# Kernel optimization log

Measured on AMD Instinct MI355X. Metric: run time of the kernel, lower is better.

## Reference

```python
import jax, jax.numpy as jnp
import numpy as np

B, T, HID = 2, 2048, 1024
NH = 8
QK_DIM = 1024
V_DIM = 2048
SCALE_BASE = 512.0
GN_EPS = 1e-5


def _xpos_rotate(x, downscale):
    # x: [B, T, QK_DIM]; XPOS rotary embedding (syncdoth/RetNet, offset=0)
    d = QK_DIM
    dh = d // 2
    pos = jnp.arange(T, dtype=jnp.float32)
    # per-pair magnitude scale
    base_scale = (jnp.arange(0, d, 2, dtype=jnp.float32) + 0.4 * d) / (1.4 * d)  # [dh]
    scale = base_scale[None, :] ** (pos[:, None] / SCALE_BASE)  # [T, dh]
    if downscale:
        scale = 1.0 / scale
    inv_freq = 1.0 / (10000.0 ** (jnp.arange(dh, dtype=jnp.float32) / dh))
    sinusoid = pos[:, None] * inv_freq[None, :]  # [T, dh]
    sin = jnp.sin(sinusoid) * scale
    cos = jnp.cos(sinusoid) * scale
    # duplicate_interleave -> [T, d]
    sin = jnp.repeat(sin, 2, axis=-1)
    cos = jnp.repeat(cos, 2, axis=-1)
    x1 = x[..., 0::2]
    x2 = x[..., 1::2]
    rot = jnp.stack((-x2, x1), axis=-1).reshape(x.shape)  # rotate_every_two
    return x * cos[None] + rot * sin[None]


def setup_inputs() -> dict:
    key = jax.random.key(0)
    k1, k2, k3, k4 = jax.random.split(key, 4)
    x = jax.random.normal(k1, (B, T, HID), dtype=jnp.float32)
    Wqkv = jax.random.normal(k2, (HID, 2 * QK_DIM + V_DIM), dtype=jnp.float32) / np.sqrt(HID)
    Wg = jax.random.normal(k3, (HID, V_DIM), dtype=jnp.float32) / np.sqrt(HID)
    Wp = jax.random.normal(k4, (V_DIM, HID), dtype=jnp.float32) / np.sqrt(V_DIM)
    bp = jnp.zeros((HID,), dtype=jnp.float32)
    return {"x": x, "Wqkv": Wqkv, "Wg": Wg, "Wp": Wp, "bp": bp}


def reference(x, Wqkv, Wg, Wp, bp):
    # multi-scale decay (non-default gamma path)
    gamma = 1.0 - jnp.exp(jnp.linspace(np.log(1.0 / 32), np.log(1.0 / 512), NH)).astype(jnp.float32)  # [NH]

    qkv = x @ Wqkv  # [B,T,2qk+v]
    q, k, v = jnp.split(qkv, [QK_DIM, 2 * QK_DIM], axis=-1)
    q = _xpos_rotate(q, downscale=False)
    k = _xpos_rotate(k, downscale=True)

    dqk = QK_DIM // NH
    dv = V_DIM // NH
    q = q.reshape(B, T, NH, dqk).transpose(0, 2, 1, 3)  # [B,H,T,dqk]
    k = k.reshape(B, T, NH, dqk).transpose(0, 2, 1, 3)
    v = v.reshape(B, T, NH, dv).transpose(0, 2, 1, 3)   # [B,H,T,dv]

    # parallel decay mask: gamma^(i-j) for i>=j else 0  -> [H,T,T]
    idx = jnp.arange(T)
    expo = idx[:, None] - idx[None, :]
    expo_safe = jnp.where(expo >= 0, expo, 0).astype(jnp.float32)
    decay_mask = jnp.where(expo[None] >= 0, gamma[:, None, None] ** expo_safe[None], 0.0)  # [H,T,T]

    scores = jnp.einsum('bhid,bhjd->bhij', q, k) * (dqk ** -0.5)
    retention = jnp.einsum('bhij,bhjv->bhiv', scores * decay_mask[None], v)  # [B,H,T,dv]

    # current_kv state: sum_t decay_mask[h,-1,t] * k_t (outer) v_t  -> [B,H,dqk,dv]
    curr_kv = jnp.einsum('bhtk,bhtv,ht->bhkv', k, v, decay_mask[:, -1, :])

    ret = retention.transpose(0, 2, 1, 3).reshape(B, T, V_DIM)

    # GroupNorm(num_groups=NH, affine=False) over [B*T, V_DIM]
    g = ret.reshape(B, T, NH, dv)
    mu = jnp.mean(g, axis=-1, keepdims=True)
    var = jnp.var(g, axis=-1, keepdims=True)
    normed = ((g - mu) / jnp.sqrt(var + GN_EPS)).reshape(B, T, V_DIM)

    gate = jax.nn.silu(x @ Wg)
    out = (gate * normed) @ Wp + bp
    return out, curr_kv
```

## Files before the change

kernel.cpp:

```cpp
#include <hip/hip_runtime.h>

typedef unsigned short u16;
typedef unsigned int   u32;
typedef unsigned long long u64;

typedef __attribute__((ext_vector_type(8))) short bf8_t;
typedef __attribute__((ext_vector_type(4))) float f4_t;

#define DEVI __device__ __forceinline__
#define MFMA16(a,b,c) __builtin_amdgcn_mfma_f32_16x16x32_bf16((a),(b),(c),0,0,0)

#define BB   2
#define TT   2048
#define HIDN 1024
#define L0f  (-3.4657359027997265f)
#define DLf  (-0.3960841031714215f)
#define SCL  (0.08838834764831845f)

DEVI u16 f2b(float f) {
    u32 u = __float_as_uint(f);
    u += 0x7FFFu + ((u >> 16) & 1u);
    return (u16)(u >> 16);
}
DEVI float b2f(u16 u) { return __uint_as_float(((u32)u) << 16); }

DEVI void gll16(const void* g, void* l) {
    __builtin_amdgcn_global_load_lds((const __attribute__((address_space(1))) void*)g,
                                     (__attribute__((address_space(3))) void*)l, 16, 0, 0);
}

__global__ __launch_bounds__(256) void k_tables(u32* __restrict__ cqp, u32* __restrict__ ckp,
                                                float* __restrict__ gt, float* __restrict__ gk) {
    int bx = blockIdx.x;
    if (bx >= 4096) {
        int i = (bx - 4096) * 256 + threadIdx.x;
        if (i < 16384) {
            int h = i >> 11, t = i & 2047;
            float lg2 = log2f(1.f - expf(L0f + (float)h * DLf));
            gt[i] = exp2f((float)(2047 - t) * lg2);
        } else {
            int idx = i - 16384;
            int h = idx >> 6, d = idx & 63;
            float lg2 = log2f(1.f - expf(L0f + (float)h * DLf));
            gk[idx] = exp2f(-(float)d * lg2);
        }
        return;
    }
    int idx = bx * 256 + threadIdx.x;
    int t = idx >> 9, m = idx & 511;
    float base = (2.f * (float)m + 409.6f) * (1.f / 1433.6f);
    float s = exp2f(log2f(base) * ((float)t * (1.f / 512.f)));
    float invf = exp2f(-(float)m * (13.287712379549449f / 512.f));
    float sn, cs;
    sincosf((float)t * invf, &sn, &cs);
    int h = m >> 6;
    float lg2h = log2f(1.f - expf(L0f + (float)h * DLf));
    float qf = s * SCL * exp2f((float)(t & 63) * lg2h);
    cqp[idx] = (u32)f2b(cs * qf) | ((u32)f2b(sn * qf) << 16);
    float is = 1.f / s;
    ckp[idx] = (u32)f2b(cs * is) | ((u32)f2b(sn * is) << 16);
}

__global__ __launch_bounds__(256) void k_cvt(const float* __restrict__ in, u16* __restrict__ out) {
    int i = blockIdx.x * 256 + threadIdx.x;
    float4 v = ((const float4*)in)[i];
    u64 pk = (u64)f2b(v.x) | ((u64)f2b(v.y) << 16) | ((u64)f2b(v.z) << 32) | ((u64)f2b(v.w) << 48);
    ((u64*)out)[i] = pk;
}

__global__ __launch_bounds__(256) void k_tposeF(const float* __restrict__ Wqkv,
                                                const float* __restrict__ Wg,
                                                const float* __restrict__ Wp,
                                                u16* __restrict__ oQ, u16* __restrict__ oG,
                                                u16* __restrict__ oP) {
    __shared__ float tile[32][33];
    int bx = blockIdx.x;
    const float* in; u16* out; int R, C, cx, ry;
    if (bx < 4096)      { in = Wqkv; out = oQ; R = 1024; C = 4096; cx = bx & 127;        ry = bx >> 7; }
    else if (bx < 6144) { int b2 = bx - 4096; in = Wg; out = oG; R = 1024; C = 2048; cx = b2 & 63; ry = b2 >> 6; }
    else                { int b2 = bx - 6144; in = Wp; out = oP; R = 2048; C = 1024; cx = b2 & 31; ry = b2 >> 5; }
    int c0 = cx * 32, r0 = ry * 32;
    int tx = threadIdx.x, ty = threadIdx.y;
#pragma unroll
    for (int i = 0; i < 4; i++)
        tile[ty * 4 + i][tx] = in[(size_t)(r0 + ty * 4 + i) * C + c0 + tx];
    __syncthreads();
#pragma unroll
    for (int i = 0; i < 4; i++)
        out[(size_t)(c0 + ty * 4 + i) * R + r0 + tx] = f2b(tile[tx][ty * 4 + i]);
}

DEVI void stage_tile(const u16* __restrict__ A, const u16* __restrict__ B,
                     int m0, int n0, int kt, char* buf, int tid, int wid) {
#pragma unroll
    for (int q = 0; q < 4; q++) {
        int flat = q * 8192 + tid * 16;
        int row = flat >> 7, byt = (flat & 127) ^ ((row & 7) << 4);
        gll16((const char*)A + (size_t)(m0 + row) * 2048 + kt * 128 + byt,
              buf + q * 8192 + wid * 1024);
        gll16((const char*)B + (size_t)(n0 + row) * 2048 + kt * 128 + byt,
              buf + 32768 + q * 8192 + wid * 1024);
    }
}

#define QPHASE(kk, fmh, LOADB)                                                        \
    {                                                                                 \
        bf8_t a_[4];                                                                  \
        _Pragma("unroll")                                                             \
        for (int f = 0; f < 4; f++) {                                                 \
            int ra = 128 * wr + ((fmh) * 4 + f) * 16 + lr;                            \
            a_[f] = *(const bf8_t*)(bA + ra * 128 + (((kk) * 64 + lg * 16) ^ ((ra & 7) << 4))); \
        }                                                                             \
        if (LOADB) {                                                                  \
            _Pragma("unroll")                                                         \
            for (int f = 0; f < 4; f++) {                                             \
                int rb = 64 * wc + f * 16 + lr;                                       \
                breg[f] = *(const bf8_t*)(bB + rb * 128 + (((kk) * 64 + lg * 16) ^ ((rb & 7) << 4))); \
            }                                                                         \
        }                                                                             \
        __builtin_amdgcn_s_barrier();                                                 \
        __builtin_amdgcn_s_setprio(1);                                                \
        _Pragma("unroll")                                                             \
        for (int f = 0; f < 4; f++)                                                   \
            _Pragma("unroll")                                                         \
            for (int j = 0; j < 4; j++)                                               \
                acc[(fmh) * 4 + f][j] = MFMA16(a_[f], breg[j], acc[(fmh) * 4 + f][j]); \
        __builtin_amdgcn_s_setprio(0);                                                \
        __builtin_amdgcn_s_barrier();                                                 \
    }

__global__ __launch_bounds__(512, 2) void k_gemm_qkvg8(
    const u16* __restrict__ xb, const u16* __restrict__ Wcat,
    const u32* __restrict__ cqp, const u32* __restrict__ ckp, const float* __restrict__ gkt,
    u16* __restrict__ qw, u16* __restrict__ kw, u16* __restrict__ kT, u16* __restrict__ vT,
    u16* __restrict__ gateb) {
    __shared__ __align__(16) char L[131072];
    int flat = blockIdx.x;
    int swz = (flat & 7) * 48 + (flat >> 3);
    int m0 = (swz / 24) * 256, n0 = (swz % 24) * 256;
    int tid = threadIdx.x, lane = tid & 63, wid = tid >> 6;
    int wr = wid >> 2, wc = wid & 3, lr = lane & 15, lg = lane >> 4;
    f4_t acc[8][4];
#pragma unroll
    for (int i = 0; i < 8; i++)
#pragma unroll
        for (int j = 0; j < 4; j++)
#pragma unroll
            for (int e = 0; e < 4; e++) acc[i][j][e] = 0.f;
    stage_tile(xb, Wcat, m0, n0, 0, L, tid, wid);
    asm volatile("s_waitcnt vmcnt(0)" ::: "memory");
    __builtin_amdgcn_s_barrier();
    for (int kt = 0; kt < 16; ++kt) {
        const char* bA = L + (kt & 1) * 65536;
        const char* bB = bA + 32768;
        if (kt < 15) {
            stage_tile(xb, Wcat, m0, n0, kt + 1, L + ((kt + 1) & 1) * 65536, tid, wid);
            asm volatile("s_waitcnt vmcnt(8)" ::: "memory");
        } else {
            asm volatile("s_waitcnt vmcnt(0)" ::: "memory");
        }
        __builtin_amdgcn_s_barrier();
        bf8_t breg[4];
        QPHASE(0, 0, 1)
        QPHASE(0, 1, 0)
        QPHASE(1, 0, 1)
        QPHASE(1, 1, 0)
    }
    char* SP = L;
    int b = m0 >> 11, t0 = m0 & 2047;
    if (n0 < 4096 && n0 >= 2048) {
        int h = (n0 - 2048) >> 8;
#pragma unroll
        for (int fm = 0; fm < 8; fm++)
#pragma unroll
            for (int fn = 0; fn < 4; fn++) {
                int dv = wc * 64 + fn * 16 + lr;
                int rowb = wr * 128 + fm * 16 + lg * 4;
                u64 pk = 0;
#pragma unroll
                for (int r = 0; r < 4; r++) pk |= ((u64)f2b(acc[fm][fn][r])) << (16 * r);
                *(u64*)(SP + dv * 512 + ((rowb * 2) ^ ((dv & 15) << 4))) = pk;
            }
        __syncthreads();
#pragma unroll
        for (int it = 0; it < 16; it++) {
            int chunk = it * 512 + tid;
            int dv = chunk >> 5, j = chunk & 31;
            uint4 v = *(const uint4*)(SP + dv * 512 + ((j * 16) ^ ((dv & 15) << 4)));
            *(uint4*)(vT + ((size_t)((b * 8 + h) * 256 + dv)) * 2048 + t0 + j * 8) = v;
        }
    } else if (n0 < 2048) {
        int isK = n0 >= 1024;
        const u32* cT = isK ? ckp : cqp;
        int hb = (n0 >> 7) & 7;
#pragma unroll
        for (int fm = 0; fm < 8; fm++)
#pragma unroll
            for (int fn = 0; fn < 4; fn++) {
                int col = wc * 64 + fn * 16 + lr;
                int gq = (n0 & 1023) + col;
                int mi = gq >> 1, h = gq >> 7;
                u64 pk = 0;
#pragma unroll
                for (int r = 0; r < 4; r++) {
                    int rowl = wr * 128 + fm * 16 + lg * 4 + r;
                    int t = t0 + rowl;
                    float v = acc[fm][fn][r];
                    float pv = __shfl_xor(v, 1);
                    u32 cp = cT[t * 512 + mi];
                    float cs = b2f((u16)cp), sn = b2f((u16)(cp >> 16));
                    float o = (col & 1) ? (v * cs + pv * sn) : (v * cs - pv * sn);
                    if (isK) {
                        pk |= ((u64)f2b(o)) << (16 * r);
                        o *= gkt[h * 64 + (t & 63)];
                    }
                    *(u16*)(SP + rowl * 512 + ((col * 2) ^ ((rowl & 15) << 4))) = f2b(o);
                }
                if (isK)
                    *(u64*)&kT[((size_t)((b * 8 + h) * 128 + (gq & 127))) * 2048 + t0 + wr * 128 + fm * 16 + lg * 4] = pk;
            }
        __syncthreads();
#pragma unroll
        for (int it = 0; it < 16; it++) {
            int chunk = it * 512 + tid;
            int r = chunk >> 5, j = chunk & 31;
            uint4 v = *(const uint4*)(SP + r * 512 + ((j * 16) ^ ((r & 15) << 4)));
            int hh = hb + (j >> 4);
            u16* g = (isK ? kw : qw) + ((size_t)((b * 8 + hh) * 2048 + t0 + r)) * 128 + (j & 15) * 8;
            *(uint4*)g = v;
        }
    } else {
        int c0 = n0 - 4096;
#pragma unroll
        for (int fm = 0; fm < 8; fm++)
#pragma unroll
            for (int fn = 0; fn < 4; fn++) {
                int col = wc * 64 + fn * 16 + lr;
#pragma unroll
                for (int r = 0; r < 4; r++) {
                    int rowl = wr * 128 + fm * 16 + lg * 4 + r;
                    float gg = acc[fm][fn][r];
                    *(u16*)(SP + rowl * 512 + ((col * 2) ^ ((rowl & 15) << 4))) = f2b(gg / (1.f + expf(-gg)));
                }
            }
        __syncthreads();
#pragma unroll
        for (int it = 0; it < 16; it++) {
            int chunk = it * 512 + tid;
            int r = chunk >> 5, j = chunk & 31;
            uint4 v = *(const uint4*)(SP + r * 512 + ((j * 16) ^ ((r & 15) << 4)));
            *(uint4*)(gateb + (size_t)(b * 2048 + t0 + r) * 2048 + c0 + j * 8) = v;
        }
    }
}

DEVI void gemm_ml(const u16* __restrict__ Ag, const u16* __restrict__ Bg, int Klen, int Kstr,
                  int m0, int n0, u16* As, u16* Bs, f4_t acc[4][4]) {
    int tid = threadIdx.x, lane = tid & 63, wid = tid >> 6;
    int wr = wid >> 1, wc = wid & 1, lr = lane & 15, lg = lane >> 4;
    for (int k0 = 0; k0 < Klen; k0 += 64) {
        __syncthreads();
#pragma unroll
        for (int p = 0; p < 4; p++) {
            int flat = p * 4096 + tid * 16;
            int row = flat >> 7, byt = (flat & 127) ^ ((row & 7) << 4);
            gll16((const char*)Ag + ((size_t)(m0 + row) * Kstr + k0) * 2 + byt,
                  (char*)As + p * 4096 + wid * 1024);
            gll16((const char*)Bg + ((size_t)(n0 + row) * Kstr + k0) * 2 + byt,
                  (char*)Bs + p * 4096 + wid * 1024);
        }
        __syncthreads();
#pragma unroll
        for (int kk = 0; kk < 2; kk++) {
            bf8_t a[4], b[4];
#pragma unroll
            for (int f = 0; f < 4; f++) {
                int ra = wr * 64 + f * 16 + lr;
                a[f] = *(const bf8_t*)((const char*)As + ra * 128 + ((kk * 64 + lg * 16) ^ ((ra & 7) << 4)));
                int rb = wc * 64 + f * 16 + lr;
                b[f] = *(const bf8_t*)((const char*)Bs + rb * 128 + ((kk * 64 + lg * 16) ^ ((rb & 7) << 4)));
            }
#pragma unroll
            for (int i = 0; i < 4; i++)
#pragma unroll
                for (int j = 0; j < 4; j++)
                    acc[i][j] = MFMA16(a[i], b[j], acc[i][j]);
        }
    }
}

DEVI void acc_zero(f4_t acc[4][4]) {
#pragma unroll
    for (int i = 0; i < 4; i++)
#pragma unroll
        for (int j = 0; j < 4; j++)
#pragma unroll
            for (int e = 0; e < 4; e++) acc[i][j][e] = 0.f;
}

__global__ __launch_bounds__(256) void k_gemm_outp(const u16* __restrict__ gdb, const u16* __restrict__ Wt,
                                                   float* __restrict__ part) {
    __shared__ u16 SM[128 * 128];
    f4_t acc[4][4]; acc_zero(acc);
    int m0 = blockIdx.y * 128, n0 = blockIdx.x * 128, kz = blockIdx.z;
    gemm_ml(gdb + kz * 1024, Wt + kz * 1024, 1024, 2048, m0, n0, SM, SM + 128 * 64, acc);
    int tid = threadIdx.x, lane = tid & 63, wid = tid >> 6;
    int wr = wid >> 1, wc = wid & 1, lr = lane & 15, lg = lane >> 4;
    float* SMf = (float*)SM;
    float* po = part + (size_t)kz * 4096 * 1024;
    __syncthreads();
#pragma unroll
    for (int p = 0; p < 2; p++) {
        if (p) __syncthreads();
        if (wr == p) {
#pragma unroll
            for (int fm = 0; fm < 4; fm++)
#pragma unroll
                for (int fn = 0; fn < 4; fn++) {
                    int col = wc * 64 + fn * 16 + lr;
#pragma unroll
                    for (int r = 0; r < 4; r++) {
                        int rowl = fm * 16 + lg * 4 + r;
                        *(float*)((char*)SMf + rowl * 512 + ((col * 4) ^ ((rowl & 7) << 6))) = acc[fm][fn][r];
                    }
                }
        }
        __syncthreads();
#pragma unroll
        for (int it2 = 0; it2 < 8; it2++) {
            int chunk = it2 * 256 + tid;
            int rowl = chunk >> 5, j = chunk & 31;
            f4_t v = *(const f4_t*)((const char*)SMf + rowl * 512 + ((j * 16) ^ ((rowl & 7) << 6)));
            *(f4_t*)((char*)po + ((size_t)(m0 + p * 64 + rowl) * 1024 + n0) * 4 + j * 16) = v;
        }
    }
}

__global__ __launch_bounds__(256) void k_outred(const float* __restrict__ part, const float* __restrict__ bp,
                                                float* __restrict__ outp) {
    int i = blockIdx.x * 256 + threadIdx.x;
    f4_t a = ((const f4_t*)part)[i];
    f4_t c = ((const f4_t*)(part + (size_t)4096 * 1024))[i];
    f4_t bb = *(const f4_t*)(bp + ((i * 4) & 1023));
#pragma unroll
    for (int e = 0; e < 4; e++) a[e] += c[e] + bb[e];
    ((f4_t*)outp)[i] = a;
}

__global__ __launch_bounds__(256, 3) void k_retention(const u16* __restrict__ qws, const u16* __restrict__ kws,
                                                      const u16* __restrict__ vTws,
                                                      u16* __restrict__ ret0, u16* __restrict__ ret1) {
    __shared__ u16 SMr[64 * 128 + 256 * 64];
    u16* Ks = SMr;
    u16* Vs = SMr + 64 * 128;
    int x = blockIdx.x;
    int it, jlo, jhi, toret1;
    if (x < 16)      { it = 15 - x;  jlo = 0;              jhi = it + 1;         toret1 = 0; }
    else if (x < 32) { it = x;       jlo = 0;              jhi = (it + 2) >> 1;  toret1 = 0; }
    else             { it = x - 16;  jlo = (it + 2) >> 1;  jhi = it + 1;         toret1 = 1; }
    int h = blockIdx.y, b = blockIdx.z;
    int bh = b * 8 + h;
    float lg2 = log2f(1.f - expf(L0f + (float)h * DLf));
    int i0 = it * 64;
    const u16* qbase = qws + (size_t)bh * 2048 * 128;
    const u16* kbase = kws + (size_t)bh * 2048 * 128;
    const u16* vbase = vTws + (size_t)bh * 256 * 2048;
    int tid = threadIdx.x, lane = tid & 63, w = tid >> 6, lr = lane & 15, lg = lane >> 4;
    bf8_t aq[4];
#pragma unroll
    for (int kk = 0; kk < 4; kk++)
        aq[kk] = *(const bf8_t*)((const char*)qbase + (size_t)(i0 + w * 16 + lr) * 256 + kk * 64 + lg * 16);
    f4_t racc[16];
#pragma unroll
    for (int f = 0; f < 16; f++)
#pragma unroll
        for (int e = 0; e < 4; e++) racc[f][e] = 0.f;
    for (int jt = jlo; jt < jhi; jt++) {
        int j0 = jt * 64;
        int diag = (jt == it);
        float tf = exp2f(64.f * (float)(it - jt) * lg2);
        __syncthreads();
#pragma unroll
        for (int p = 0; p < 4; p++) {
            int flat = p * 4096 + tid * 16;
            int row = flat >> 8, byt = (flat & 255) ^ ((row & 7) << 4);
            gll16((const char*)kbase + (size_t)(j0 + row) * 256 + byt, (char*)Ks + p * 4096 + w * 1024);
        }
#pragma unroll
        for (int p = 0; p < 8; p++) {
            int flat = p * 4096 + tid * 16;
            int row = flat >> 7, byt = (flat & 127) ^ ((row & 7) << 4);
            gll16((const char*)vbase + (size_t)row * 4096 + (size_t)j0 * 2 + byt,
                  (char*)Vs + p * 4096 + w * 1024);
        }
        __syncthreads();
        f4_t sacc[4];
#pragma unroll
        for (int f = 0; f < 4; f++)
#pragma unroll
            for (int e = 0; e < 4; e++) sacc[f][e] = 0.f;
#pragma unroll
        for (int kk = 0; kk < 4; kk++)
#pragma unroll
            for (int fn = 0; fn < 4; fn++) {
                int rb = fn * 16 + lr;
                bf8_t bb = *(const bf8_t*)((const char*)Ks + rb * 256 + ((kk * 64 + lg * 16) ^ ((rb & 7) << 4)));
                sacc[fn] = MFMA16(aq[kk], bb, sacc[fn]);
            }
        __syncthreads();
#pragma unroll
        for (int fn = 0; fn < 4; fn++)
#pragma unroll
            for (int r = 0; r < 4; r++) {
                int i_loc = w * 16 + lg * 4 + r;
                int col = fn * 16 + lr;
                float v = diag ? ((i_loc - col >= 0) ? sacc[fn][r] : 0.f) : sacc[fn][r] * tf;
                *(u16*)((char*)Ks + i_loc * 128 + ((col * 2) ^ ((i_loc & 7) << 4))) = f2b(v);
            }
#pragma unroll
        for (int kk = 0; kk < 2; kk++) {
            int ra = w * 16 + lr;
            bf8_t ap = *(const bf8_t*)((const char*)Ks + ra * 128 + ((kk * 64 + lg * 16) ^ ((ra & 7) << 4)));
#pragma unroll
            for (int fn2 = 0; fn2 < 16; fn2++) {
                int rb = fn2 * 16 + lr;
                bf8_t bv = *(const bf8_t*)((const char*)Vs + rb * 128 + ((kk * 64 + lg * 16) ^ ((rb & 7) << 4)));
                racc[fn2] = MFMA16(ap, bv, racc[fn2]);
            }
        }
    }
    __syncthreads();
    u16* St = Vs;
#pragma unroll
    for (int fn2 = 0; fn2 < 16; fn2++)
#pragma unroll
        for (int r = 0; r < 4; r++) {
            int il = w * 16 + lg * 4 + r;
            int dv = fn2 * 16 + lr;
            *(u16*)((char*)St + il * 512 + ((dv * 2) ^ ((il & 15) << 4))) = f2b(racc[fn2][r]);
        }
    __syncthreads();
#pragma unroll
    for (int it2 = 0; it2 < 8; it2++) {
        int chunk = it2 * 256 + tid;
        int il = chunk >> 5, j = chunk & 31;
        uint4 v = *(const uint4*)((const char*)St + il * 512 + ((j * 16) ^ ((il & 15) << 4)));
        char* dst;
        if (toret1) dst = (char*)ret1 + ((size_t)(b * 1024 + i0 - 1024 + il) * 2048 + h * 256) * 2 + j * 16;
        else        dst = (char*)ret0 + ((size_t)(b * 2048 + i0 + il) * 2048 + h * 256) * 2 + j * 16;
        *(uint4*)dst = v;
    }
}

__global__ __launch_bounds__(512) void k_currkv(const u16* __restrict__ kTws, const u16* __restrict__ vTws,
                                                const float* __restrict__ gtab, float* __restrict__ part) {
    __shared__ u16 Ks2[128 * 64];
    __shared__ u16 Vws[256 * 64];
    int tr = blockIdx.x;
    int bh = blockIdx.y;
    int h = bh & 7;
    const u16* kT = kTws + (size_t)bh * 128 * 2048;
    const u16* vT = vTws + (size_t)bh * 256 * 2048;
    const float* gt = gtab + h * 2048;
    int tid = threadIdx.x, lane = tid & 63, wid = tid >> 6;
    int wr = wid >> 2, wc = wid & 3, lr = lane & 15, lg = lane >> 4;
    f4_t acc[4][4]; acc_zero(acc);
    for (int tc = 0; tc < 8; tc++) {
        int t0 = tr * 512 + tc * 64;
        __syncthreads();
#pragma unroll
        for (int p = 0; p < 2; p++) {
            int flat = p * 8192 + tid * 16;
            int row = flat >> 7, byt = (flat & 127) ^ ((row & 7) << 4);
            gll16((const char*)kT + (size_t)row * 4096 + (size_t)t0 * 2 + byt,
                  (char*)Ks2 + p * 8192 + wid * 1024);
        }
#pragma unroll
        for (int p = 0; p < 4; p++) {
            int flat = p * 8192 + tid * 16;
            int row = flat >> 7, byt = flat & 127;
            int tt = t0 + (byt >> 1);
            const u16* src = vT + (size_t)row * 2048 + tt;
            u16 tmp[8]; *(uint4*)tmp = *(const uint4*)src;
            const float* gp = gt + tt;
            u16 op[8];
#pragma unroll
            for (int e = 0; e < 8; e++) op[e] = f2b(b2f(tmp[e]) * gp[e]);
            *(uint4*)((char*)Vws + row * 128 + (byt ^ ((row & 7) << 4))) = *(uint4*)op;
        }
        __syncthreads();
#pragma unroll
        for (int kk = 0; kk < 2; kk++) {
            bf8_t a[4], bb[4];
#pragma unroll
            for (int f = 0; f < 4; f++) {
                int ra = wr * 64 + f * 16 + lr;
                a[f] = *(const bf8_t*)((const char*)Ks2 + ra * 128 + ((kk * 64 + lg * 16) ^ ((ra & 7) << 4)));
                int rb = wc * 64 + f * 16 + lr;
                bb[f] = *(const bf8_t*)((const char*)Vws + rb * 128 + ((kk * 64 + lg * 16) ^ ((rb & 7) << 4)));
            }
#pragma unroll
            for (int i = 0; i < 4; i++)
#pragma unroll
                for (int j = 0; j < 4; j++)
                    acc[i][j] = MFMA16(a[i], bb[j], acc[i][j]);
        }
    }
#pragma unroll
    for (int fm = 0; fm < 4; fm++)
#pragma unroll
        for (int fn = 0; fn < 4; fn++)
#pragma unroll
            for (int r = 0; r < 4; r++) {
                int dk = wr * 64 + fm * 16 + lg * 4 + r;
                int dv = wc * 64 + fn * 16 + lr;
                part[((size_t)(bh * 4 + tr)) * 32768 + (size_t)dk * 256 + dv] = acc[fm][fn][r];
            }
}

__global__ __launch_bounds__(256) void k_reduce_ckv(const float* __restrict__ part, float* __restrict__ outc) {
    int i = blockIdx.x * 256 + threadIdx.x;
    int bh = i >> 15, wv = i & 32767;
    float s = 0.f;
#pragma unroll
    for (int tr = 0; tr < 4; tr++) s += part[((size_t)(bh * 4 + tr)) * 32768 + wv];
    outc[i] = s;
}

__global__ __launch_bounds__(256) void k_gnorm(const u16* __restrict__ ret0, const u16* __restrict__ ret1,
                                               const u16* __restrict__ gateb, u16* __restrict__ gatedb) {
    int g = blockIdx.x * 4 + (threadIdx.x >> 6);
    int lane = threadIdx.x & 63;
    int row = g >> 3, h = g & 7;
    size_t base = (size_t)row * 2048 + h * 256 + lane * 4;
    u64 p0 = *(const u64*)(ret0 + base);
    float e0 = b2f((u16)p0), e1 = b2f((u16)(p0 >> 16)), e2 = b2f((u16)(p0 >> 32)), e3 = b2f((u16)(p0 >> 48));
    if ((row & 2047) >= 1024) {
        size_t b1 = (size_t)((row >> 11) * 1024 + (row & 1023)) * 2048 + h * 256 + lane * 4;
        u64 p1 = *(const u64*)(ret1 + b1);
        e0 += b2f((u16)p1); e1 += b2f((u16)(p1 >> 16)); e2 += b2f((u16)(p1 >> 32)); e3 += b2f((u16)(p1 >> 48));
    }
    float s = e0 + e1 + e2 + e3;
    float sqs = e0 * e0 + e1 * e1 + e2 * e2 + e3 * e3;
#pragma unroll
    for (int m = 1; m < 64; m <<= 1) { s += __shfl_xor(s, m); sqs += __shfl_xor(sqs, m); }
    float mean = s * (1.f / 256.f);
    float var = sqs * (1.f / 256.f) - mean * mean;
    float inv = rsqrtf(var + 1e-5f);
    u64 gp = *(const u64*)(gateb + base);
    u64 pk = (u64)f2b((e0 - mean) * inv * b2f((u16)gp)) |
             ((u64)f2b((e1 - mean) * inv * b2f((u16)(gp >> 16))) << 16) |
             ((u64)f2b((e2 - mean) * inv * b2f((u16)(gp >> 32))) << 32) |
             ((u64)f2b((e3 - mean) * inv * b2f((u16)(gp >> 48))) << 48);
    *(u64*)(gatedb + base) = pk;
}

extern "C" void kernel_launch(void* const* d_in, const int* in_sizes, int n_in,
                              void* d_out, int out_size, void* d_ws, size_t ws_size,
                              hipStream_t stream) {
    const float* x    = (const float*)d_in[0];
    const float* Wqkv = (const float*)d_in[1];
    const float* Wg   = (const float*)d_in[2];
    const float* Wp   = (const float*)d_in[3];
    const float* bp   = (const float*)d_in[4];
    float* outp   = (float*)d_out;
    float* outckv = outp + (size_t)BB * TT * HIDN;

    char* ws = (char*)d_ws;
    const size_t MB = 1024 * 1024;
    u16*   xb     = (u16*)(ws);
    u16*   WqkvT  = (u16*)(ws + 8 * MB);
    u16*   WgT    = (u16*)(ws + 16 * MB);
    u16*   WpT    = (u16*)(ws + 20 * MB);
    u32*   cqp    = (u32*)(ws + 24 * MB);
    u32*   ckp    = (u32*)(ws + 28 * MB);
    u16*   gateb  = (u16*)(ws + 32 * MB);
    u16*   qw     = (u16*)(ws + 48 * MB);
    u16*   kw     = (u16*)(ws + 56 * MB);
    u16*   kT     = (u16*)(ws + 64 * MB);
    u16*   vT     = (u16*)(ws + 72 * MB);
    u16*   ret0b  = (u16*)(ws + 88 * MB);
    u16*   ret1b  = (u16*)(ws + 104 * MB);
    float* ckvp   = (float*)(ws + 112 * MB);
    float* gtab   = (float*)(ws + 120 * MB);
    float* gkt    = (float*)(ws + 120 * MB + 65536);
    u16*   gatedb = (u16*)(ws + 48 * MB);
    float* opart  = (float*)(ws + 88 * MB);

    hipLaunchKernelGGL(k_tables, dim3(4162), dim3(256), 0, stream, cqp, ckp, gtab, gkt);
    hipLaunchKernelGGL(k_cvt, dim3(4096), dim3(256), 0, stream, x, xb);
    hipLaunchKernelGGL(k_tposeF, dim3(8192), dim3(32, 8), 0, stream, Wqkv, Wg, Wp, WqkvT, WgT, WpT);
    hipLaunchKernelGGL(k_gemm_qkvg8, dim3(384), dim3(512), 0, stream,
                       xb, WqkvT, cqp, ckp, gkt, qw, kw, kT, vT, gateb);
    hipLaunchKernelGGL(k_currkv, dim3(4, 16), dim3(512), 0, stream, kT, vT, gtab, ckvp);
    hipLaunchKernelGGL(k_reduce_ckv, dim3(2048), dim3(256), 0, stream, ckvp, outckv);
    hipLaunchKernelGGL(k_retention, dim3(48, 8, 2), dim3(256), 0, stream, qw, kw, vT, ret0b, ret1b);
    hipLaunchKernelGGL(k_gnorm, dim3(8192), dim3(256), 0, stream, ret0b, ret1b, gateb, gatedb);
    hipLaunchKernelGGL(k_gemm_outp, dim3(8, 32, 2), dim3(256), 0, stream, gatedb, WpT, opart);
    hipLaunchKernelGGL(k_outred, dim3(4096), dim3(256), 0, stream, opart, bp, outp);
}
```

Before: 228.4 us.

## Interleave next-tile global loads across MFMA phases in QKV/gate GEMM

Splits per-k-tile staging into eight chunk loads and spreads them across the four MFMA compute phases instead of issuing them all up front. Waits are finer-grained (vmcnt(2)) and chunk order is arranged so the first phase's A rows and B tile land early. This aims to overlap global-to-LDS traffic with matrix math and cut stall time at each tile boundary. The tighter barrier/waitcnt choreography makes correctness depend on the exact chunk ordering.

```diff
diff --git a/kernel.cpp b/kernel.cpp
--- a/kernel.cpp
+++ b/kernel.cpp
@@ -90,20 +90,20 @@
         out[(size_t)(c0 + ty * 4 + i) * R + r0 + tx] = f2b(tile[tx][ty * 4 + i]);
 }
 
-DEVI void stage_tile(const u16* __restrict__ A, const u16* __restrict__ B,
-                     int m0, int n0, int kt, char* buf, int tid, int wid) {
-#pragma unroll
-    for (int q = 0; q < 4; q++) {
-        int flat = q * 8192 + tid * 16;
-        int row = flat >> 7, byt = (flat & 127) ^ ((row & 7) << 4);
+DEVI void stage_chunk(const u16* __restrict__ A, const u16* __restrict__ B,
+                      int m0, int n0, int kt, char* buf, int id, int wid, int lane) {
+    int j = id & 3;
+    int flat = j * 8192 + wid * 1024 + lane * 16;
+    int row = flat >> 7, byt = (flat & 127) ^ ((row & 7) << 4);
+    if (id < 4)
         gll16((const char*)A + (size_t)(m0 + row) * 2048 + kt * 128 + byt,
-              buf + q * 8192 + wid * 1024);
+              buf + j * 8192 + wid * 1024);
+    else
         gll16((const char*)B + (size_t)(n0 + row) * 2048 + kt * 128 + byt,
-              buf + 32768 + q * 8192 + wid * 1024);
-    }
-}
-
-#define QPHASE(kk, fmh, LOADB)                                                        \
+              buf + 32768 + j * 8192 + wid * 1024);
+}
+
+#define QCORE(kk, fmh, LOADB)                                                         \
     {                                                                                 \
         bf8_t a_[4];                                                                  \
         _Pragma("unroll")                                                             \
@@ -126,7 +126,6 @@
             for (int j = 0; j < 4; j++)                                               \
                 acc[(fmh) * 4 + f][j] = MFMA16(a_[f], breg[j], acc[(fmh) * 4 + f][j]); \
         __builtin_amdgcn_s_setprio(0);                                                \
-        __builtin_amdgcn_s_barrier();                                                 \
     }
 
 __global__ __launch_bounds__(512, 2) void k_gemm_qkvg8(
@@ -147,25 +146,50 @@
         for (int j = 0; j < 4; j++)
 #pragma unroll
             for (int e = 0; e < 4; e++) acc[i][j][e] = 0.f;
-    stage_tile(xb, Wcat, m0, n0, 0, L, tid, wid);
-    asm volatile("s_waitcnt vmcnt(0)" ::: "memory");
+    stage_chunk(xb, Wcat, m0, n0, 0, L, 0, wid, lane);
+    stage_chunk(xb, Wcat, m0, n0, 0, L, 2, wid, lane);
+    stage_chunk(xb, Wcat, m0, n0, 0, L, 4, wid, lane);
+    stage_chunk(xb, Wcat, m0, n0, 0, L, 5, wid, lane);
+    stage_chunk(xb, Wcat, m0, n0, 0, L, 6, wid, lane);
+    stage_chunk(xb, Wcat, m0, n0, 0, L, 7, wid, lane);
+    stage_chunk(xb, Wcat, m0, n0, 0, L, 1, wid, lane);
+    stage_chunk(xb, Wcat, m0, n0, 0, L, 3, wid, lane);
+    asm volatile("s_waitcnt vmcnt(2)" ::: "memory");
     __builtin_amdgcn_s_barrier();
     for (int kt = 0; kt < 16; ++kt) {
         const char* bA = L + (kt & 1) * 65536;
         const char* bB = bA + 32768;
+        char* nbuf = L + ((kt + 1) & 1) * 65536;
+        bf8_t breg[4];
         if (kt < 15) {
-            stage_tile(xb, Wcat, m0, n0, kt + 1, L + ((kt + 1) & 1) * 65536, tid, wid);
-            asm volatile("s_waitcnt vmcnt(8)" ::: "memory");
-        } else {
-            asm volatile("s_waitcnt vmcnt(0)" ::: "memory");
-        }
+            stage_chunk(xb, Wcat, m0, n0, kt + 1, nbuf, 0, wid, lane);
+            stage_chunk(xb, Wcat, m0, n0, kt + 1, nbuf, 2, wid, lane);
+        }
+        QCORE(0, 0, 1)
+        if (kt < 15) { asm volatile("s_waitcnt vmcnt(2)" ::: "memory"); }
+        else         { asm volatile("s_waitcnt vmcnt(0)" ::: "memory"); }
         __builtin_amdgcn_s_barrier();
-        bf8_t breg[4];
-        QPHASE(0, 0, 1)
-        QPHASE(0, 1, 0)
-        QPHASE(1, 0, 1)
-        QPHASE(1, 1, 0)
-    }
+        if (kt < 15) {
+            stage_chunk(xb, Wcat, m0, n0, kt + 1, nbuf, 4, wid, lane);
+            stage_chunk(xb, Wcat, m0, n0, kt + 1, nbuf, 5, wid, lane);
+        }
+        QCORE(0, 1, 0)
+        __builtin_amdgcn_s_barrier();
+        if (kt < 15) {
+            stage_chunk(xb, Wcat, m0, n0, kt + 1, nbuf, 6, wid, lane);
+            stage_chunk(xb, Wcat, m0, n0, kt + 1, nbuf, 7, wid, lane);
+        }
+        QCORE(1, 0, 1)
+        __builtin_amdgcn_s_barrier();
+        if (kt < 15) {
+            stage_chunk(xb, Wcat, m0, n0, kt + 1, nbuf, 1, wid, lane);
+            stage_chunk(xb, Wcat, m0, n0, kt + 1, nbuf, 3, wid, lane);
+        }
+        QCORE(1, 1, 0)
+        if (kt < 15) { asm volatile("s_waitcnt vmcnt(2)" ::: "memory"); }
+        __builtin_amdgcn_s_barrier();
+    }
+    __syncthreads();
     char* SP = L;
     int b = m0 >> 11, t0 = m0 & 2047;
     if (n0 < 4096 && n0 >= 2048) {
```

Result: no change. 225.8 us (-1.1%).
